# Performance work log

Hardware: AMD Instinct MI355X
Metric: run time of the kernel (lower is better)

The kernel has to match this reference:

```python
import jax, jax.numpy as jnp
import numpy as np

MSE_W, SSIM_W = 0.6, 0.4
WIN, SIGMA = 11, 1.5


def _gaussian_window():
    coords = jnp.arange(WIN, dtype=jnp.float32) - (WIN - 1) / 2.0
    g = jnp.exp(-coords ** 2 / (2.0 * SIGMA ** 2))
    g = g / g.sum()
    w = jnp.outer(g, g)  # [11,11]
    return w.reshape(1, 1, WIN, WIN)  # OIHW


def _blur(x, window):
    # x: [B,1,H,W], valid conv with 11x11 gaussian
    return jax.lax.conv_general_dilated(
        x, window, window_strides=(1, 1), padding='VALID',
        dimension_numbers=('NCHW', 'OIHW', 'NCHW'))


def setup_inputs() -> dict:
    key = jax.random.key(0)
    k1, k2 = jax.random.split(key)
    pred = jax.random.uniform(k1, (32, 1, 512, 512), dtype=jnp.float32)
    target = jax.random.uniform(k2, (32, 1, 512, 512), dtype=jnp.float32)
    return {"pred": pred, "target": target}


def reference(pred, target):
    window = _gaussian_window()
    C1 = (0.01 * 1.0) ** 2
    C2 = (0.03 * 1.0) ** 2

    mse_loss = jnp.mean((pred - target) ** 2)

    mu1 = _blur(pred, window)
    mu2 = _blur(target, window)
    mu1_sq = mu1 * mu1
    mu2_sq = mu2 * mu2
    mu1_mu2 = mu1 * mu2
    sigma1_sq = _blur(pred * pred, window) - mu1_sq
    sigma2_sq = _blur(target * target, window) - mu2_sq
    sigma12 = _blur(pred * target, window) - mu1_mu2

    ssim_map = (2.0 * mu1_mu2 + C1) * (2.0 * sigma12 + C2) / (
        (mu1_sq + mu2_sq + C1) * (sigma1_sq + sigma2_sq + C2) + 1e-6)
    ssim_loss = 1.0 - jnp.mean(ssim_map)

    return MSE_W * mse_loss + SSIM_W * ssim_loss
```

## Files before the change

### kernel.cpp

```cpp
#include <hip/hip_runtime.h>
#include <math.h>

#define BATCH 32
#define H 512
#define W 512
#define OUT_HW 502
#define TS_X 32
#define BAND 32
#define NBANDS 4
#define STRIP (BAND * NBANDS)
#define NTX 16
#define NSTRIP 4
#define NBLOCKS (NTX * NSTRIP * BATCH)
#define N1 ((double)BATCH * H * W)
#define N2 ((double)BATCH * OUT_HW * OUT_HW)

struct GaussW { float g[11]; };

typedef _Float16 h8  __attribute__((ext_vector_type(8)));
typedef __fp16   h2t __attribute__((ext_vector_type(2)));
typedef float    f4t __attribute__((ext_vector_type(4)));

__global__ __launch_bounds__(256, 2)
void ssim_mfma_kernel(const float* __restrict__ pred,
                      const float* __restrict__ targ,
                      float* __restrict__ ws_contrib,
                      GaussW gw)
{
    __shared__ __align__(16) _Float16 raw[4][48 * 48];
    __shared__ __align__(16) _Float16 rbt[4][32 * 48];
    __shared__ float red[8];

    const int tid = threadIdx.x;
    const int tx = blockIdx.x, sy = blockIdx.y, b = blockIdx.z;
    const int ox0 = tx * TS_X;
    const int S = sy * STRIP;
    const int cols = min(TS_X, OUT_HW - ox0);
    const int mse_end = S + STRIP;
    const bool interior_x = (ox0 + 48 <= W);

    const float* __restrict__ pb = pred + ((size_t)b << 18);
    const float* __restrict__ tb = targ + ((size_t)b << 18);

    const int lane = tid & 63, wave = tid >> 6;
    const int quad = lane >> 4, nn = lane & 15, quad8 = quad << 3;

    const int pr = tid / 6, pg = tid - pr * 6;
    const bool pactive = interior_x | (pg < 4);

    {
        _Float16* base = &raw[0][0];
        const int total = 4 * 48 * 48;
        for (int i = tid * 8; i < total; i += 256 * 8)
            *(f4t*)(base + i) = f4t{0.f, 0.f, 0.f, 0.f};
    }

    h8 gfrag;
    #pragma unroll
    for (int j = 0; j < 8; ++j) {
        const int kk = quad8 + j - nn;
        float val = 0.f;
        #pragma unroll
        for (int t2 = 0; t2 < 11; ++t2) val = (kk == t2) ? gw.g[t2] : val;
        gfrag[j] = (_Float16)val;
    }
    const f4t zero4 = {0.f, 0.f, 0.f, 0.f};
    const float C1 = 1e-4f, C2 = 9e-4f;

    float mse_local = 0.f, ssim_local = 0.f;

    f4t pf0, pf1, pf2, pf3;
    {
        const int h0 = S, nnew = min(S + 42, H) - h0;
        if ((tid < nnew * 6) & pactive) {
            const int base = ((h0 + pr) << 9) + ox0 + 8 * pg;
            pf0 = *(const f4t*)(pb + base);
            pf1 = *(const f4t*)(pb + base + 4);
            pf2 = *(const f4t*)(tb + base);
            pf3 = *(const f4t*)(tb + base + 4);
        }
    }

    __syncthreads();

    #pragma unroll 1
    for (int band = 0; band < NBANDS; ++band) {
        const int out0 = S + band * BAND;
        const int h0   = (band == 0) ? S : (out0 + 10);
        const int nnew = min(out0 + 42, H) - h0;

        if ((tid < nnew * 6) & pactive) {
            const int gy = h0 + pr;
            const h2t hp0 = __builtin_amdgcn_cvt_pkrtz(pf0[0], pf0[1]);
            const h2t hp1 = __builtin_amdgcn_cvt_pkrtz(pf0[2], pf0[3]);
            const h2t hp2 = __builtin_amdgcn_cvt_pkrtz(pf1[0], pf1[1]);
            const h2t hp3 = __builtin_amdgcn_cvt_pkrtz(pf1[2], pf1[3]);
            const h2t ht0 = __builtin_amdgcn_cvt_pkrtz(pf2[0], pf2[1]);
            const h2t ht1 = __builtin_amdgcn_cvt_pkrtz(pf2[2], pf2[3]);
            const h2t ht2 = __builtin_amdgcn_cvt_pkrtz(pf3[0], pf3[1]);
            const h2t ht3 = __builtin_amdgcn_cvt_pkrtz(pf3[2], pf3[3]);
            __align__(16) h2t sv[4], dv[4], ssv[4], ddv[4];
            sv[0] = hp0 + ht0; sv[1] = hp1 + ht1; sv[2] = hp2 + ht2; sv[3] = hp3 + ht3;
            dv[0] = hp0 - ht0; dv[1] = hp1 - ht1; dv[2] = hp2 - ht2; dv[3] = hp3 - ht3;
            ssv[0] = sv[0] * sv[0]; ssv[1] = sv[1] * sv[1];
            ssv[2] = sv[2] * sv[2]; ssv[3] = sv[3] * sv[3];
            ddv[0] = dv[0] * dv[0]; ddv[1] = dv[1] * dv[1];
            ddv[2] = dv[2] * dv[2]; ddv[3] = dv[3] * dv[3];

            if ((pg < 4) & (gy < mse_end)) {
                const h2t macc = (ddv[0] + ddv[1]) + (ddv[2] + ddv[3]);
                mse_local += (float)macc[0] + (float)macc[1];
            }

            int u = gy - S;
            u -= (u >= 96) ? 96 : ((u >= 48) ? 48 : 0);
            const int off = u * 48 + 8 * pg;
            *(f4t*)&raw[0][off] = *(const f4t*)sv;
            *(f4t*)&raw[1][off] = *(const f4t*)dv;
            *(f4t*)&raw[2][off] = *(const f4t*)ssv;
            *(f4t*)&raw[3][off] = *(const f4t*)ddv;
        }
        __syncthreads();

        if (band + 1 < NBANDS) {
            const int nout0 = S + (band + 1) * BAND;
            const int nh0   = nout0 + 10;
            const int nnnew = min(nout0 + 42, H) - nh0;
            if ((tid < nnnew * 6) & pactive) {
                const int base = ((nh0 + pr) << 9) + ox0 + 8 * pg;
                pf0 = *(const f4t*)(pb + base);
                pf1 = *(const f4t*)(pb + base + 4);
                pf2 = *(const f4t*)(tb + base);
                pf3 = *(const f4t*)(tb + base + 4);
            }
        }

        #pragma unroll 1
        for (int t5 = wave; t5 < 24; t5 += 4) {
            const int ch = t5 & 3, rem = t5 >> 2;
            const int j0 = (rem & 1) << 4, r0 = (rem >> 1) << 4;
            int u = band * BAND + r0 + nn;
            u -= (u >= 96) ? 96 : ((u >= 48) ? 48 : 0);
            const h8 a = *(const h8*)&raw[ch][u * 48 + j0 + quad8];
            const f4t dacc = __builtin_amdgcn_mfma_f32_16x16x32_f16(a, gfrag, zero4, 0, 0, 0);
            h2t* wp = (h2t*)&rbt[ch][(j0 + nn) * 48 + r0 + (quad << 2)];
            wp[0] = __builtin_amdgcn_cvt_pkrtz(dacc[0], dacc[1]);
            wp[1] = __builtin_amdgcn_cvt_pkrtz(dacc[2], dacc[3]);
        }
        __syncthreads();

        {
            const int c0 = (wave & 1) << 4, r0v = (wave >> 1) << 4;
            f4t dv2[4];
            #pragma unroll
            for (int ch = 0; ch < 4; ++ch) {
                const h8 a = *(const h8*)&rbt[ch][(c0 + nn) * 48 + r0v + quad8];
                dv2[ch] = __builtin_amdgcn_mfma_f32_16x16x32_f16(a, gfrag, zero4, 0, 0, 0);
            }
            const int rowg = out0 + r0v + nn;
            if (rowg < OUT_HW) {
                #pragma unroll
                for (int reg = 0; reg < 4; ++reg) {
                    const int cl = c0 + (quad << 2) + reg;
                    if (cl < cols) {
                        const float A = dv2[0][reg], Bv = dv2[1][reg];
                        const float U = dv2[2][reg], V  = dv2[3][reg];
                        const float A2 = A * A, B2 = Bv * Bv;
                        const float mu12_2 = 0.5f * (A2 - B2);
                        const float musq   = 0.5f * (A2 + B2);
                        const float sig12_2 = 0.5f * (U - V) - mu12_2;
                        const float sigsum  = 0.5f * (U + V) - musq;
                        const float num = (mu12_2 + C1) * (sig12_2 + C2);
                        const float den = (musq + C1) * (sigsum + C2) + 1e-6f;
                        ssim_local += num * __builtin_amdgcn_rcpf(den);
                    }
                }
            }
        }
    }

    #pragma unroll
    for (int off = 32; off > 0; off >>= 1) {
        ssim_local += __shfl_down(ssim_local, off, 64);
        mse_local  += __shfl_down(mse_local,  off, 64);
    }
    if ((tid & 63) == 0) { red[wave] = ssim_local; red[4 + wave] = mse_local; }
    __syncthreads();
    if (tid == 0) {
        const float s = red[0] + red[1] + red[2] + red[3];
        const float m = red[4] + red[5] + red[6] + red[7];
        const double contrib = 0.6 * (double)m / N1 - 0.4 * (double)s / N2;
        const int bid = (b * NSTRIP + sy) * NTX + tx;
        ws_contrib[bid] = (float)contrib;
    }
}

__global__ __launch_bounds__(1024)
void finalize_kernel(const float* __restrict__ ws_contrib,
                     float* __restrict__ out)
{
    __shared__ double rs[1024];
    int tid = threadIdx.x;
    double s = 0.0;
    for (int i = tid; i < NBLOCKS; i += 1024)
        s += (double)ws_contrib[i];
    rs[tid] = s;
    __syncthreads();
    for (int off = 512; off > 0; off >>= 1) {
        if (tid < off) rs[tid] += rs[tid + off];
        __syncthreads();
    }
    if (tid == 0)
        out[0] = (float)(0.4 + rs[0]);
}

extern "C" void kernel_launch(void* const* d_in, const int* in_sizes, int n_in,
                              void* d_out, int out_size, void* d_ws, size_t ws_size,
                              hipStream_t stream)
{
    const float* pred = (const float*)d_in[0];
    const float* targ = (const float*)d_in[1];
    float* out = (float*)d_out;
    float* ws_contrib = (float*)d_ws;

    GaussW gw;
    double g[11], sum = 0.0;
    for (int i = 0; i < 11; ++i) { double x = i - 5.0; g[i] = exp(-x * x / 4.5); sum += g[i]; }
    for (int i = 0; i < 11; ++i) gw.g[i] = (float)(g[i] / sum);

    ssim_mfma_kernel<<<dim3(NTX, NSTRIP, BATCH), 256, 0, stream>>>(pred, targ, ws_contrib, gw);
    finalize_kernel<<<1, 1024, 0, stream>>>(ws_contrib, out);
}
```

Baseline: 108.9 us.

## Process full image height per block to eliminate strip halo reloads

```diff
diff --git a/kernel.cpp b/kernel.cpp
--- a/kernel.cpp
+++ b/kernel.cpp
@@ -7,11 +7,9 @@
 #define OUT_HW 502
 #define TS_X 32
 #define BAND 32
-#define NBANDS 4
-#define STRIP (BAND * NBANDS)
+#define NBANDS 16
 #define NTX 16
-#define NSTRIP 4
-#define NBLOCKS (NTX * NSTRIP * BATCH)
+#define NBLOCKS (NTX * BATCH)
 #define N1 ((double)BATCH * H * W)
 #define N2 ((double)BATCH * OUT_HW * OUT_HW)
 
@@ -32,11 +30,11 @@
     __shared__ float red[8];
 
     const int tid = threadIdx.x;
-    const int tx = blockIdx.x, sy = blockIdx.y, b = blockIdx.z;
+    const int bid = blockIdx.x;
+    const int tx  = bid >> 5;
+    const int b   = ((bid & 7) << 2) | ((bid >> 3) & 3);
     const int ox0 = tx * TS_X;
-    const int S = sy * STRIP;
     const int cols = min(TS_X, OUT_HW - ox0);
-    const int mse_end = S + STRIP;
     const bool interior_x = (ox0 + 48 <= W);
 
     const float* __restrict__ pb = pred + ((size_t)b << 18);
@@ -71,9 +69,9 @@
 
     f4t pf0, pf1, pf2, pf3;
     {
-        const int h0 = S, nnew = min(S + 42, H) - h0;
+        const int nnew = 42;
         if ((tid < nnew * 6) & pactive) {
-            const int base = ((h0 + pr) << 9) + ox0 + 8 * pg;
+            const int base = (pr << 9) + ox0 + 8 * pg;
             pf0 = *(const f4t*)(pb + base);
             pf1 = *(const f4t*)(pb + base + 4);
             pf2 = *(const f4t*)(tb + base);
@@ -83,14 +81,15 @@
 
     __syncthreads();
 
+    int hbase = 0, obase = 0;
+
     #pragma unroll 1
     for (int band = 0; band < NBANDS; ++band) {
-        const int out0 = S + band * BAND;
-        const int h0   = (band == 0) ? S : (out0 + 10);
+        const int out0 = band * BAND;
+        const int h0   = (band == 0) ? 0 : (out0 + 10);
         const int nnew = min(out0 + 42, H) - h0;
 
         if ((tid < nnew * 6) & pactive) {
-            const int gy = h0 + pr;
             const h2t hp0 = __builtin_amdgcn_cvt_pkrtz(pf0[0], pf0[1]);
             const h2t hp1 = __builtin_amdgcn_cvt_pkrtz(pf0[2], pf0[3]);
             const h2t hp2 = __builtin_amdgcn_cvt_pkrtz(pf1[0], pf1[1]);
@@ -107,14 +106,14 @@
             ddv[0] = dv[0] * dv[0]; ddv[1] = dv[1] * dv[1];
             ddv[2] = dv[2] * dv[2]; ddv[3] = dv[3] * dv[3];
 
-            if ((pg < 4) & (gy < mse_end)) {
+            if (pg < 4) {
                 const h2t macc = (ddv[0] + ddv[1]) + (ddv[2] + ddv[3]);
                 mse_local += (float)macc[0] + (float)macc[1];
             }
 
-            int u = gy - S;
-            u -= (u >= 96) ? 96 : ((u >= 48) ? 48 : 0);
-            const int off = u * 48 + 8 * pg;
+            int s = hbase + pr;
+            s -= (s >= 48) ? 48 : 0;
+            const int off = s * 48 + 8 * pg;
             *(f4t*)&raw[0][off] = *(const f4t*)sv;
             *(f4t*)&raw[1][off] = *(const f4t*)dv;
             *(f4t*)&raw[2][off] = *(const f4t*)ssv;
@@ -123,9 +122,8 @@
         __syncthreads();
 
         if (band + 1 < NBANDS) {
-            const int nout0 = S + (band + 1) * BAND;
-            const int nh0   = nout0 + 10;
-            const int nnnew = min(nout0 + 42, H) - nh0;
+            const int nh0   = out0 + BAND + 10;
+            const int nnnew = min(out0 + BAND + 42, H) - nh0;
             if ((tid < nnnew * 6) & pactive) {
                 const int base = ((nh0 + pr) << 9) + ox0 + 8 * pg;
                 pf0 = *(const f4t*)(pb + base);
@@ -139,8 +137,8 @@
         for (int t5 = wave; t5 < 24; t5 += 4) {
             const int ch = t5 & 3, rem = t5 >> 2;
             const int j0 = (rem & 1) << 4, r0 = (rem >> 1) << 4;
-            int u = band * BAND + r0 + nn;
-            u -= (u >= 96) ? 96 : ((u >= 48) ? 48 : 0);
+            int u = obase + r0 + nn;
+            u -= (u >= 48) ? 48 : 0;
             const h8 a = *(const h8*)&raw[ch][u * 48 + j0 + quad8];
             const f4t dacc = __builtin_amdgcn_mfma_f32_16x16x32_f16(a, gfrag, zero4, 0, 0, 0);
             h2t* wp = (h2t*)&rbt[ch][(j0 + nn) * 48 + r0 + (quad << 2)];
@@ -177,6 +175,9 @@
                 }
             }
         }
+
+        hbase += nnew;  hbase -= (hbase >= 48) ? 48 : 0;
+        obase += BAND;  obase -= (obase >= 48) ? 48 : 0;
     }
 
     #pragma unroll
@@ -190,7 +191,6 @@
         const float s = red[0] + red[1] + red[2] + red[3];
         const float m = red[4] + red[5] + red[6] + red[7];
         const double contrib = 0.6 * (double)m / N1 - 0.4 * (double)s / N2;
-        const int bid = (b * NSTRIP + sy) * NTX + tx;
         ws_contrib[bid] = (float)contrib;
     }
 }
@@ -228,6 +228,6 @@
     for (int i = 0; i < 11; ++i) { double x = i - 5.0; g[i] = exp(-x * x / 4.5); sum += g[i]; }
     for (int i = 0; i < 11; ++i) gw.g[i] = (float)(g[i] / sum);
 
-    ssim_mfma_kernel<<<dim3(NTX, NSTRIP, BATCH), 256, 0, stream>>>(pred, targ, ws_contrib, gw);
+    ssim_mfma_kernel<<<dim3(NBLOCKS), 256, 0, stream>>>(pred, targ, ws_contrib, gw);
     finalize_kernel<<<1, 1024, 0, stream>>>(ws_contrib, out);
 }
```

After: 108.7 us. About the same (-0.2%).
